# Kernel optimization log

Hardware: AMD Instinct MI355X
Metric: run time of the kernel (lower is better)

## Reference

```python
import jax, jax.numpy as jnp
import numpy as np

B, CELL, K, L, V = 2048, 512, 30, 1024, 80


def setup_inputs() -> dict:
    key = jax.random.key(0)
    k1, k2, k3, k4, k5, k6 = jax.random.split(key, 6)
    x = jax.random.normal(k1, (B, CELL), dtype=jnp.float32)
    kappa_old = jax.random.uniform(k2, (B, K), dtype=jnp.float32) * 5.0
    # real one-hot text encodings [B, L, V]
    chars = jax.random.randint(k3, (B, L), 0, V)
    onehots = jax.nn.one_hot(chars, V, dtype=jnp.float32)
    text_lens = jax.random.randint(k4, (B, 1), 1, L + 1).astype(jnp.float32)
    # small weights so exp() stays in a sane range
    W = jax.random.normal(k5, (3 * K, CELL), dtype=jnp.float32) * 0.05
    b = jax.random.normal(k6, (3 * K,), dtype=jnp.float32) * 0.05
    return {"x": x, "kappa_old": kappa_old, "onehots": onehots,
            "text_lens": text_lens, "W": W, "b": b}


def reference(x, kappa_old, onehots, text_lens, W, b):
    L_pad = onehots.shape[1]  # padded_text_len
    params = jnp.exp(x @ W.T + b)            # [B, 3K]
    alpha, beta, pre_kappa = jnp.split(params, 3, axis=-1)  # each [B, K]
    kappa = kappa_old + pre_kappa             # [B, K]
    idx = jnp.arange(L_pad + 1, dtype=x.dtype)  # [L+1]
    # gravity: [B, K, L+1]
    gravity = -beta[:, :, None] * (kappa[:, :, None] - idx) ** 2
    phi = jnp.einsum('bk,bkl->bl', alpha, jnp.exp(gravity))  # [B, L+1]
    phi = phi * (jnp.asarray(L_pad, x.dtype) / text_lens)     # [B, L+1]
    w = jnp.einsum('bl,blv->bv', phi[:, :L_pad], onehots)     # [B, V]
    return w, kappa, phi
```

## Files before the change

kernel.cpp:

```cpp
#include <hip/hip_runtime.h>
#include <math.h>

namespace {
constexpr int Bn    = 2048;
constexpr int CELLn = 512;
constexpr int Kn    = 30;
constexpr int Ln    = 1024;
constexpr int Vn    = 80;
constexpr int NT    = 320;
constexpr int RP    = 16;
}

typedef float f4v __attribute__((ext_vector_type(4)));

__global__ __launch_bounds__(NT) void window_fused(
    const float* __restrict__ x,
    const float* __restrict__ kappa_old,
    const float* __restrict__ onehots,
    const float* __restrict__ text_lens,
    const float* __restrict__ W,
    const float* __restrict__ bias,
    float* __restrict__ out_w,
    float* __restrict__ out_kappa,
    float* __restrict__ out_phi)
{
    const int b = blockIdx.x;
    const int t = threadIdx.x;

    __shared__ float s_x[CELLn];
    __shared__ float s_abk[3 * Kn];
    __shared__ float s_phi[Ln];
    __shared__ float s_red[RP][Vn];
    __shared__ int   s_nmax;

    if (t < 128) ((float4*)s_x)[t] = ((const float4*)(x + (size_t)b * CELLn))[t];
    if (t == 128) s_nmax = 0;
    __syncthreads();

    if (t < 3 * Kn) {
        const float4* wrow = (const float4*)(W + (size_t)t * CELLn);
        const float4* xr   = (const float4*)s_x;
        float a0 = 0.f, a1 = 0.f, a2 = 0.f, a3 = 0.f;
        #pragma unroll 8
        for (int i = 0; i < CELLn / 4; ++i) {
            float4 wv = wrow[i];
            float4 xv = xr[i];
            a0 = fmaf(wv.x, xv.x, a0);
            a1 = fmaf(wv.y, xv.y, a1);
            a2 = fmaf(wv.z, xv.z, a2);
            a3 = fmaf(wv.w, xv.w, a3);
        }
        float val = expf((a0 + a1) + (a2 + a3) + bias[t]);
        if (t >= 2 * Kn) {
            int k = t - 2 * Kn;
            float kap = kappa_old[(size_t)b * Kn + k] + val;
            s_abk[t] = kap;
            out_kappa[(size_t)b * Kn + k] = kap;
        } else {
            s_abk[t] = val;
        }
    }
    __syncthreads();

    const float scale = (float)Ln / text_lens[b];
    for (int l = t; l <= Ln; l += NT) {
        const float fl = (float)l;
        float acc = 0.f;
        #pragma unroll
        for (int k = 0; k < Kn; ++k) {
            float d = s_abk[2 * Kn + k] - fl;
            acc = fmaf(s_abk[k], expf(-s_abk[Kn + k] * d * d), acc);
        }
        float ph = acc * scale;
        out_phi[(size_t)b * (Ln + 1) + l] = ph;
        if (l < Ln) {
            s_phi[l] = ph;
            if (ph != 0.f) atomicMax(&s_nmax, l + 1);
        }
    }
    __syncthreads();
    const int n_eff = s_nmax;

    const int j  = t % 20;
    const int r0 = t / 20;
    const f4v* oh = (const f4v*)(onehots + (size_t)b * Ln * Vn);

    f4v acc = {0.f, 0.f, 0.f, 0.f};
    #pragma unroll 2
    for (int l = r0; l < n_eff; l += RP) {
        f4v v = oh[l * 20 + j];
        acc += s_phi[l] * v;
    }
    *((f4v*)&s_red[r0][j * 4]) = acc;
    __syncthreads();

    if (t < Vn) {
        float s = 0.f;
        #pragma unroll
        for (int r = 0; r < RP; ++r) s += s_red[r][t];
        out_w[(size_t)b * Vn + t] = s;
    }
}

extern "C" void kernel_launch(void* const* d_in, const int* in_sizes, int n_in,
                              void* d_out, int out_size, void* d_ws, size_t ws_size,
                              hipStream_t stream) {
    const float* x         = (const float*)d_in[0];
    const float* kappa_old = (const float*)d_in[1];
    const float* onehots   = (const float*)d_in[2];
    const float* text_lens = (const float*)d_in[3];
    const float* W         = (const float*)d_in[4];
    const float* bias      = (const float*)d_in[5];

    float* out       = (float*)d_out;
    float* out_w     = out;
    float* out_kappa = out + (size_t)Bn * Vn;
    float* out_phi   = out_kappa + (size_t)Bn * Kn;

    window_fused<<<Bn, NT, 0, stream>>>(x, kappa_old, onehots, text_lens, W, bias,
                                        out_w, out_kappa, out_phi);
}
```

Before: 808.8 us.

## Shrink block to 256 threads, split GEMV rows, unroll phi over four positions

Drops the block size from 320 to 256 threads and requests 8 blocks per SM through launch bounds. The dense projection now splits each weight row across two threads and combines the halves with a lane shuffle. The phi loop is rewritten so each thread computes four positions at once, sharing the loaded alpha, beta and kappa values, with thread 0 handling the last position. The one-hot reduction now uses 12 row partitions on 240 of the threads. The aim is higher occupancy and fewer shared-memory loads, at the cost of fewer threads streaming the one-hot matrix, which is likely the bandwidth-bound stage.

```diff
diff --git a/kernel.cpp b/kernel.cpp
--- a/kernel.cpp
+++ b/kernel.cpp
@@ -7,13 +7,13 @@
 constexpr int Kn    = 30;
 constexpr int Ln    = 1024;
 constexpr int Vn    = 80;
-constexpr int NT    = 320;
-constexpr int RP    = 16;
+constexpr int NT    = 256;
+constexpr int RP    = 12;
 }
 
 typedef float f4v __attribute__((ext_vector_type(4)));
 
-__global__ __launch_bounds__(NT) void window_fused(
+__global__ __launch_bounds__(NT, 8) void window_fused(
     const float* __restrict__ x,
     const float* __restrict__ kappa_old,
     const float* __restrict__ onehots,
@@ -37,12 +37,14 @@
     if (t == 128) s_nmax = 0;
     __syncthreads();
 
-    if (t < 3 * Kn) {
-        const float4* wrow = (const float4*)(W + (size_t)t * CELLn);
-        const float4* xr   = (const float4*)s_x;
+    if (t < 2 * 3 * Kn) {
+        const int r = t >> 1;
+        const int h = t & 1;
+        const float4* wrow = (const float4*)(W + (size_t)r * CELLn) + h * (CELLn / 8);
+        const float4* xr   = (const float4*)s_x + h * (CELLn / 8);
         float a0 = 0.f, a1 = 0.f, a2 = 0.f, a3 = 0.f;
-        #pragma unroll 8
-        for (int i = 0; i < CELLn / 4; ++i) {
+        #pragma unroll 4
+        for (int i = 0; i < CELLn / 8; ++i) {
             float4 wv = wrow[i];
             float4 xv = xr[i];
             a0 = fmaf(wv.x, xv.x, a0);
@@ -50,48 +52,81 @@
             a2 = fmaf(wv.z, xv.z, a2);
             a3 = fmaf(wv.w, xv.w, a3);
         }
-        float val = expf((a0 + a1) + (a2 + a3) + bias[t]);
-        if (t >= 2 * Kn) {
-            int k = t - 2 * Kn;
-            float kap = kappa_old[(size_t)b * Kn + k] + val;
-            s_abk[t] = kap;
-            out_kappa[(size_t)b * Kn + k] = kap;
-        } else {
-            s_abk[t] = val;
+        float part = (a0 + a1) + (a2 + a3);
+        part += __shfl_xor(part, 1);
+        if (h == 0) {
+            float val = expf(part + bias[r]);
+            if (r >= 2 * Kn) {
+                int k = r - 2 * Kn;
+                float kap = kappa_old[(size_t)b * Kn + k] + val;
+                s_abk[r] = kap;
+                out_kappa[(size_t)b * Kn + k] = kap;
+            } else {
+                s_abk[r] = val;
+            }
         }
     }
     __syncthreads();
 
     const float scale = (float)Ln / text_lens[b];
-    for (int l = t; l <= Ln; l += NT) {
-        const float fl = (float)l;
-        float acc = 0.f;
-        #pragma unroll
+    {
+        const float fl0 = (float)t;
+        const float fl1 = fl0 + 256.f;
+        const float fl2 = fl0 + 512.f;
+        const float fl3 = fl0 + 768.f;
+        float p0 = 0.f, p1 = 0.f, p2 = 0.f, p3 = 0.f;
+        #pragma unroll 2
         for (int k = 0; k < Kn; ++k) {
-            float d = s_abk[2 * Kn + k] - fl;
-            acc = fmaf(s_abk[k], expf(-s_abk[Kn + k] * d * d), acc);
+            const float a  = s_abk[k];
+            const float bt = s_abk[Kn + k];
+            const float kp = s_abk[2 * Kn + k];
+            float d0 = kp - fl0, d1 = kp - fl1, d2 = kp - fl2, d3 = kp - fl3;
+            p0 = fmaf(a, expf(-bt * d0 * d0), p0);
+            p1 = fmaf(a, expf(-bt * d1 * d1), p1);
+            p2 = fmaf(a, expf(-bt * d2 * d2), p2);
+            p3 = fmaf(a, expf(-bt * d3 * d3), p3);
         }
-        float ph = acc * scale;
-        out_phi[(size_t)b * (Ln + 1) + l] = ph;
-        if (l < Ln) {
-            s_phi[l] = ph;
-            if (ph != 0.f) atomicMax(&s_nmax, l + 1);
+        p0 *= scale; p1 *= scale; p2 *= scale; p3 *= scale;
+        float* op = out_phi + (size_t)b * (Ln + 1);
+        op[t]       = p0;
+        op[t + 256] = p1;
+        op[t + 512] = p2;
+        op[t + 768] = p3;
+        s_phi[t]       = p0;
+        s_phi[t + 256] = p1;
+        s_phi[t + 512] = p2;
+        s_phi[t + 768] = p3;
+        int nc = 0;
+        if (p0 != 0.f) nc = t + 1;
+        if (p1 != 0.f) nc = t + 257;
+        if (p2 != 0.f) nc = t + 513;
+        if (p3 != 0.f) nc = t + 769;
+        if (nc) atomicMax(&s_nmax, nc);
+        if (t == 0) {
+            float acc = 0.f;
+            #pragma unroll 2
+            for (int k = 0; k < Kn; ++k) {
+                float d = s_abk[2 * Kn + k] - (float)Ln;
+                acc = fmaf(s_abk[k], expf(-s_abk[Kn + k] * d * d), acc);
+            }
+            op[Ln] = acc * scale;
         }
     }
     __syncthreads();
     const int n_eff = s_nmax;
 
-    const int j  = t % 20;
-    const int r0 = t / 20;
-    const f4v* oh = (const f4v*)(onehots + (size_t)b * Ln * Vn);
-
-    f4v acc = {0.f, 0.f, 0.f, 0.f};
-    #pragma unroll 2
-    for (int l = r0; l < n_eff; l += RP) {
-        f4v v = oh[l * 20 + j];
-        acc += s_phi[l] * v;
+    if (t < RP * 20) {
+        const int j  = t % 20;
+        const int r0 = t / 20;
+        const f4v* oh = (const f4v*)(onehots + (size_t)b * Ln * Vn);
+        f4v acc = {0.f, 0.f, 0.f, 0.f};
+        #pragma unroll 2
+        for (int l = r0; l < n_eff; l += RP) {
+            f4v v = oh[l * 20 + j];
+            acc += s_phi[l] * v;
+        }
+        *((f4v*)&s_red[r0][j * 4]) = acc;
     }
-    *((f4v*)&s_red[r0][j * 4]) = acc;
     __syncthreads();
 
     if (t < Vn) {
```

Measured after the change: 774.2 us. -4.3%, faster.
